# Kernel optimization log

Measured on AMD Instinct MI355X. Metric: run time of the kernel, lower is better.

## Reference

```python
import jax, jax.numpy as jnp
import numpy as np

B, P, R, H, M, A = 2048, 2048, 4096, 6, 256, 256
TAU, BETA = 0.1, 5.0


def setup_inputs() -> dict:
    key = jax.random.key(0)
    ks = jax.random.split(key, 12)
    M_minus = jax.random.uniform(ks[0], (B, M), dtype=jnp.float32)
    # rank-0 actions as sparse binary mask over predicates
    action_mask = (jax.random.uniform(ks[1], (B, P)) < 0.01).astype(jnp.float32)
    # temporal gate per (microstep, rule): 0/1
    gate = (jax.random.uniform(ks[2], (B, R)) < 0.7).astype(jnp.float32)
    body_idx = jax.random.randint(ks[3], (R, H), 0, P, dtype=jnp.int32)
    body_mask = (jax.random.uniform(ks[4], (R, H)) < 0.6).astype(jnp.float32)
    body_mask = body_mask.at[:, 0].set(1.0)  # every rule has >=1 body atom
    head_idx = jax.random.randint(ks[5], (R,), 0, P, dtype=jnp.int32)
    mental_pos = jnp.arange(M, dtype=jnp.int32)  # mental predicates occupy first M slots
    rtype = jax.random.randint(ks[6], (R,), 0, 3)
    is_toM = (rtype <= 1).astype(jnp.float32)   # A->M or M->M rules
    is_toA = (rtype == 2).astype(jnp.float32)   # M->A rules
    Gamma_AtoM = 0.1 * jax.random.normal(ks[7], (R, M), dtype=jnp.float32)
    Gamma_MtoA = 0.1 * jax.random.normal(ks[8], (R, A), dtype=jnp.float32)
    b = -2.0 * jnp.ones((A,), dtype=jnp.float32)
    w = 0.2 * jax.random.normal(ks[9], (A, M), dtype=jnp.float32)
    return {"M_minus": M_minus, "action_mask": action_mask, "gate": gate,
            "body_mask": body_mask, "is_toM": is_toM, "is_toA": is_toA,
            "Gamma_AtoM": Gamma_AtoM, "Gamma_MtoA": Gamma_MtoA, "b": b, "w": w,
            "body_idx": body_idx, "head_idx": head_idx, "mental_pos": mental_pos}


def reference(M_minus, action_mask, gate, body_mask, is_toM, is_toA,
              Gamma_AtoM, Gamma_MtoA, b, w, body_idx, head_idx, mental_pos):
    Mclip = jnp.clip(M_minus, 0.0, 1.0)                       # [B,M]
    # build_val_for_microstep: scatter mental vals, set rank-0 actions to 1
    val = jnp.zeros((B, P), dtype=M_minus.dtype).at[:, mental_pos].set(Mclip)
    val = jnp.maximum(val, action_mask)                        # [B,P]

    # eval_clause_exact: soft-AND (soft-min, temperature tau) over body atoms
    body_vals = val[:, body_idx]                               # [B,R,H] gather
    v = jnp.where(body_mask > 0, body_vals, 1e4)               # padded slots never min
    g_body = -TAU * jax.nn.logsumexp(-v / TAU, axis=-1)        # [B,R]
    g = g_body * gate                                          # temporal gate

    # per-head clause aggregation: g_head = (1/beta) logsumexp_{r:head(r)=p} beta*g_r
    def seg_lse(gb):  # gb: [R]
        mx = jax.ops.segment_max(BETA * gb, head_idx, num_segments=P)
        mx_safe = jnp.where(mx > -1e30, mx, 0.0)
        s = jax.ops.segment_sum(jnp.exp(BETA * gb - mx_safe[head_idx]),
                                head_idx, num_segments=P)
        lse = (mx_safe + jnp.log(jnp.maximum(s, 1e-30))) / BETA
        return jnp.where(s > 0, lse, -1e9)
    g_head = jax.vmap(seg_lse)(g)                              # [B,P]

    mental_mask = jnp.zeros((P,), dtype=val.dtype).at[mental_pos].set(1.0)
    val_new = jnp.where(mental_mask > 0, jnp.maximum(val, g_head), val)

    # S_j(t) = relu(sum over A->M/M->M rules gamma_AtoM[r] * g_r)
    S = jax.nn.relu(jnp.einsum('br,rm->bm', g * is_toM, Gamma_AtoM))  # [B,M]
    # lambda_k(t) = softplus(b + w@M) + relu(sum over M->A rules gamma_MtoA[r]*g_r)
    lam_ment = jax.nn.softplus(b + Mclip @ w.T)                # [B,A]
    lam_logic = jax.nn.relu(jnp.einsum('br,ra->ba', g * is_toA, Gamma_MtoA))
    lam = lam_ment + lam_logic
    return jnp.concatenate([val_new, S, lam], axis=-1)         # [B, P+M+A]
```

## Files before the change

### kernel.cpp

```cpp
#include <hip/hip_runtime.h>

typedef __attribute__((ext_vector_type(8))) short short8;
typedef __attribute__((ext_vector_type(4))) float f32x4;

#define B_DIM 2048
#define P_DIM 2048
#define R_DIM 4096
#define H_DIM 6
#define M_DIM 256
#define A_DIM 256
#define OUT_STRIDE 2560
#define NB 2

#define C1 14.426950408889634f
#define K2 0.06931471805599453f
#define C2 7.213475204444817f
#define K3 0.13862943611198906f

static __device__ __forceinline__ float fexp2(float x) { return __builtin_amdgcn_exp2f(x); }
static __device__ __forceinline__ float flog2(float x) { return __builtin_amdgcn_logf(x); }

static __device__ __forceinline__ unsigned short f2bf(float f) {
    unsigned u = __builtin_bit_cast(unsigned, f);
    u += 0x7fffu + ((u >> 16) & 1u);
    return (unsigned short)(u >> 16);
}
static __device__ __forceinline__ float bf2f_lo(unsigned u) {
    return __builtin_bit_cast(float, u << 16);
}
static __device__ __forceinline__ float bf2f_hi(unsigned u) {
    return __builtin_bit_cast(float, u & 0xFFFF0000u);
}
static __device__ __forceinline__ unsigned short f2h(float f) {
    return __builtin_bit_cast(unsigned short, (_Float16)f);
}
static __device__ __forceinline__ float h2f(unsigned short u) {
    return (float)__builtin_bit_cast(_Float16, u);
}

__global__ __launch_bounds__(256) void prep_meta(
    const int* __restrict__ bidx, const float* __restrict__ bmask,
    const int* __restrict__ hidx, uint4* __restrict__ meta)
{
    const int r = blockIdx.x * 256 + threadIdx.x;
    const int* bi = bidx + r * H_DIM;
    const float* bm = bmask + r * H_DIM;
    unsigned s[H_DIM];
    #pragma unroll
    for (int h = 0; h < H_DIM; h++)
        s[h] = (bm[h] > 0.0f) ? (unsigned)bi[h] : 2048u;
    const int hh = hidx[r];
    unsigned sh = (hh < M_DIM) ? (unsigned)hh : 0xFFFFu;
    uint4 m;
    m.x = s[0] | (s[1] << 16);
    m.y = s[2] | (s[3] << 16);
    m.z = s[4] | (s[5] << 16);
    m.w = sh;
    meta[r] = m;
}

__global__ __launch_bounds__(1024, 8) void main_fused(
    const float* __restrict__ M_minus, const float* __restrict__ amask,
    const float* __restrict__ gate,    const uint4* __restrict__ meta,
    const float* __restrict__ GA, const float* __restrict__ GB,
    const float* __restrict__ isM, const float* __restrict__ isA,
    const float* __restrict__ w,
    unsigned short* __restrict__ GAT, unsigned short* __restrict__ GBT,
    unsigned short* __restrict__ wb,
    unsigned short* __restrict__ g_bf, unsigned short* __restrict__ mclip_bf,
    float* __restrict__ outp)
{
    __shared__ __align__(16) union SM {
        struct {
            unsigned vrowu[2052];
            float shead[NB][M_DIM];
        } mf;
        float prep[4][32][33];
    } sm;
    const int bid = blockIdx.x;
    const int tid = threadIdx.x;
    const int b0 = bid * NB;

    if (bid < 576) {
        const int s = tid >> 8, lt = tid & 255;
        const int u = bid * 4 + s;
        const int tx = lt & 31, ty = lt >> 5;
        if (u < 2048) {
            const int which = u >> 10;
            const int rem = u & 1023;
            const float* src = which ? GB : GA;
            const float* scv = which ? isA : isM;
            const int r0 = (rem >> 3) * 32;
            const int n0 = (rem & 7) * 32;
            #pragma unroll
            for (int q = 0; q < 4; q++) {
                int rr = ty + q * 8;
                sm.prep[s][rr][tx] = scv[r0 + rr] * src[(size_t)(r0 + rr) * 256 + n0 + tx];
            }
        } else {
            const int i = (u - 2048) * 256 + lt;
            wb[i] = f2bf(w[i]);
        }
        __syncthreads();
        if (u < 2048) {
            const int which = u >> 10;
            const int rem = u & 1023;
            unsigned short* dst = which ? GBT : GAT;
            const int r0 = (rem >> 3) * 32;
            const int n0 = (rem & 7) * 32;
            #pragma unroll
            for (int q = 0; q < 4; q++) {
                int nn = ty + q * 8;
                dst[(size_t)(n0 + nn) * R_DIM + r0 + tx] = f2bf(sm.prep[s][tx][nn]);
            }
        }
        __syncthreads();
    }

    if (tid < NB * M_DIM) sm.mf.shead[tid >> 8][tid & 255] = 0.0f;
    if (tid == 0) {
        unsigned sb = (unsigned)f2bf(-1.0e9f);
        sm.mf.vrowu[2048] = sb | (sb << 16);
    }

    {
        const int p0 = tid * 2;
        float2 a0 = *(const float2*)(amask + (size_t)b0 * P_DIM + p0);
        float2 a1 = *(const float2*)(amask + (size_t)(b0 + 1) * P_DIM + p0);
        if (tid < M_DIM / 2) {
            float2 m0 = *(const float2*)(M_minus + (size_t)b0 * M_DIM + p0);
            float2 m1 = *(const float2*)(M_minus + (size_t)(b0 + 1) * M_DIM + p0);
            float mc00 = fminf(fmaxf(m0.x, 0.0f), 1.0f);
            float mc01 = fminf(fmaxf(m0.y, 0.0f), 1.0f);
            float mc10 = fminf(fmaxf(m1.x, 0.0f), 1.0f);
            float mc11 = fminf(fmaxf(m1.y, 0.0f), 1.0f);
            ushort2 w0; w0.x = f2bf(mc00); w0.y = f2bf(mc01);
            ushort2 w1; w1.x = f2bf(mc10); w1.y = f2bf(mc11);
            *(ushort2*)(mclip_bf + (size_t)b0 * M_DIM + p0) = w0;
            *(ushort2*)(mclip_bf + (size_t)(b0 + 1) * M_DIM + p0) = w1;
            a0.x = fmaxf(mc00, a0.x); a0.y = fmaxf(mc01, a0.y);
            a1.x = fmaxf(mc10, a1.x); a1.y = fmaxf(mc11, a1.y);
        }
        unsigned u0 = (unsigned)f2bf(-C1 * a0.x) | ((unsigned)f2bf(-C1 * a1.x) << 16);
        unsigned u1 = (unsigned)f2bf(-C1 * a0.y) | ((unsigned)f2bf(-C1 * a1.y) << 16);
        *(uint2*)&sm.mf.vrowu[p0] = make_uint2(u0, u1);
    }
    __syncthreads();

    const float* g0p = gate + (size_t)b0 * R_DIM;
    const float* g1p = gate + (size_t)(b0 + 1) * R_DIM;
    unsigned short* o0p = g_bf + (size_t)b0 * R_DIM;
    unsigned short* o1p = g_bf + (size_t)(b0 + 1) * R_DIM;

    uint4 mc = meta[tid];
    float ga = g0p[tid], gb = g1p[tid];
    #pragma unroll
    for (int it = 0; it < R_DIM / 1024; it++) {
        const int rr = tid + it * 1024;
        uint4 mn = mc; float gan = ga, gbn = gb;
        if (it < R_DIM / 1024 - 1) {
            mn  = meta[rr + 1024];
            gan = g0p[rr + 1024];
            gbn = g1p[rr + 1024];
        }
        const int i0 = mc.x & 0xFFFF, i1 = mc.x >> 16;
        const int i2 = mc.y & 0xFFFF, i3 = mc.y >> 16;
        const int i4 = mc.z & 0xFFFF, i5 = mc.z >> 16;
        const int hh = mc.w & 0xFFFF;
        unsigned u0 = sm.mf.vrowu[i0], u1 = sm.mf.vrowu[i1], u2 = sm.mf.vrowu[i2];
        unsigned u3 = sm.mf.vrowu[i3], u4 = sm.mf.vrowu[i4], u5 = sm.mf.vrowu[i5];

        float s0 = fexp2(bf2f_lo(u0)) + fexp2(bf2f_lo(u1)) + fexp2(bf2f_lo(u2))
                 + fexp2(bf2f_lo(u3)) + fexp2(bf2f_lo(u4)) + fexp2(bf2f_lo(u5));
        float s1 = fexp2(bf2f_hi(u0)) + fexp2(bf2f_hi(u1)) + fexp2(bf2f_hi(u2))
                 + fexp2(bf2f_hi(u3)) + fexp2(bf2f_hi(u4)) + fexp2(bf2f_hi(u5));
        float gg0 = flog2(s0) * (-K2 * ga);
        float gg1 = flog2(s1) * (-K2 * gb);
        o0p[rr] = f2bf(gg0);
        o1p[rr] = f2bf(gg1);
        if (hh < M_DIM) {
            atomicAdd(&sm.mf.shead[0][hh], fexp2(gg0 * C2));
            atomicAdd(&sm.mf.shead[1][hh], fexp2(gg1 * C2));
        }
        mc = mn; ga = gan; gb = gbn;
    }
    __syncthreads();

    {
        const int p0 = tid * 2;
        uint2 uu = *(const uint2*)&sm.mf.vrowu[p0];
        float v00 = -K2 * bf2f_lo(uu.x), v10 = -K2 * bf2f_hi(uu.x);
        float v01 = -K2 * bf2f_lo(uu.y), v11 = -K2 * bf2f_hi(uu.y);
        if (tid < M_DIM / 2) {
            float s00 = sm.mf.shead[0][p0], s01 = sm.mf.shead[0][p0 + 1];
            float s10 = sm.mf.shead[1][p0], s11 = sm.mf.shead[1][p0 + 1];
            if (s00 > 0.0f) v00 = fmaxf(v00, K3 * flog2(s00));
            if (s01 > 0.0f) v01 = fmaxf(v01, K3 * flog2(s01));
            if (s10 > 0.0f) v10 = fmaxf(v10, K3 * flog2(s10));
            if (s11 > 0.0f) v11 = fmaxf(v11, K3 * flog2(s11));
        }
        *(float2*)(outp + (size_t)b0 * OUT_STRIDE + p0)       = make_float2(v00, v01);
        *(float2*)(outp + (size_t)(b0 + 1) * OUT_STRIDE + p0) = make_float2(v10, v11);
    }
}

__device__ __forceinline__ void stage16(unsigned short* lds,
                                        const unsigned short* gsrc,
                                        int K, int c)
{
    const int row = c >> 4, slot = c & 15;
    const int k8 = slot ^ (row & 15);
    __builtin_amdgcn_global_load_lds(
        (const __attribute__((address_space(1))) void*)(gsrc + (size_t)row * K + k8 * 8),
        (__attribute__((address_space(3))) void*)(lds + c * 8), 16, 0, 0);
}

__global__ __launch_bounds__(256) void gemm_all(
    const unsigned short* __restrict__ g_bf,
    const unsigned short* __restrict__ GAT,
    const unsigned short* __restrict__ mclip,
    const unsigned short* __restrict__ w_bf,
    unsigned short* __restrict__ mainp, unsigned short* __restrict__ lamp)
{
    __shared__ __align__(16) unsigned short Alds[128 * 128];
    __shared__ __align__(16) unsigned short Blds[64 * 128];
    const int bid = blockIdx.x;
    const int tid = threadIdx.x;
    const int lane = tid & 63, wid = tid >> 6;
    const int wr = wid >> 1, wc = wid & 1;

    if (bid < 512) {
        const int l = (bid & 7) * 64 + (bid >> 3);
        const int m0 = (l & 15) * 128;
        const int n0 = ((l >> 4) & 7) * 64;
        const int z  = l >> 7;
        const int K = R_DIM, Kc = R_DIM / 4, k0 = z * Kc, NS = 512;
        unsigned short* part = mainp + (size_t)z * B_DIM * NS;
        f32x4 acc[4][2] = {};

        for (int kt = 0; kt < Kc; kt += 128) {
            const unsigned short* Ab = g_bf + (size_t)m0 * K + k0 + kt;
            const unsigned short* Bb = GAT  + (size_t)n0 * K + k0 + kt;
            #pragma unroll
            for (int q = 0; q < 8; q++) stage16(Alds, Ab, K, tid + q * 256);
            #pragma unroll
            for (int q = 0; q < 4; q++) stage16(Blds, Bb, K, tid + q * 256);
            __syncthreads();
            #pragma unroll
            for (int ks = 0; ks < 4; ks++) {
                const int k8 = ks * 4 + (lane >> 4);
                const int ra = wr * 64 + (lane & 15);
                const int rb = wc * 32 + (lane & 15);
                const int sa = (k8 ^ (ra & 15)) << 3;
                const int sb = (k8 ^ (rb & 15)) << 3;
                short8 a0 = *(const short8*)&Alds[(ra)      * 128 + sa];
                short8 a1 = *(const short8*)&Alds[(ra + 16) * 128 + sa];
                short8 a2 = *(const short8*)&Alds[(ra + 32) * 128 + sa];
                short8 a3 = *(const short8*)&Alds[(ra + 48) * 128 + sa];
                short8 b0 = *(const short8*)&Blds[(rb)      * 128 + sb];
                short8 b1 = *(const short8*)&Blds[(rb + 16) * 128 + sb];
                acc[0][0] = __builtin_amdgcn_mfma_f32_16x16x32_bf16(a0, b0, acc[0][0], 0, 0, 0);
                acc[0][1] = __builtin_amdgcn_mfma_f32_16x16x32_bf16(a0, b1, acc[0][1], 0, 0, 0);
                acc[1][0] = __builtin_amdgcn_mfma_f32_16x16x32_bf16(a1, b0, acc[1][0], 0, 0, 0);
                acc[1][1] = __builtin_amdgcn_mfma_f32_16x16x32_bf16(a1, b1, acc[1][1], 0, 0, 0);
                acc[2][0] = __builtin_amdgcn_mfma_f32_16x16x32_bf16(a2, b0, acc[2][0], 0, 0, 0);
                acc[2][1] = __builtin_amdgcn_mfma_f32_16x16x32_bf16(a2, b1, acc[2][1], 0, 0, 0);
                acc[3][0] = __builtin_amdgcn_mfma_f32_16x16x32_bf16(a3, b0, acc[3][0], 0, 0, 0);
                acc[3][1] = __builtin_amdgcn_mfma_f32_16x16x32_bf16(a3, b1, acc[3][1], 0, 0, 0);
            }
            __syncthreads();
        }
        const int rbase = (lane >> 4) * 4;
        const int cbase = lane & 15;
        #pragma unroll
        for (int i = 0; i < 4; i++) {
            #pragma unroll
            for (int j = 0; j < 2; j++) {
                const int gn = n0 + wc * 32 + j * 16 + cbase;
                #pragma unroll
                for (int q = 0; q < 4; q++) {
                    const int gm = m0 + wr * 64 + i * 16 + rbase + q;
                    part[(size_t)gm * NS + gn] = f2h(acc[i][j][q]);
                }
            }
        }
    } else {
        const int l = bid - 512;
        const int m0 = (l & 31) * 64;
        const int n0 = ((l >> 5) & 3) * 64;
        const int z  = l >> 7;
        const int K = M_DIM, Kc = M_DIM / 2, k0 = z * Kc, NS = A_DIM;
        unsigned short* part = lamp + (size_t)z * B_DIM * NS;
        f32x4 acc[2][2] = {};

        const unsigned short* Ab = mclip + (size_t)m0 * K + k0;
        const unsigned short* Bb = w_bf  + (size_t)n0 * K + k0;
        #pragma unroll
        for (int q = 0; q < 4; q++) {
            stage16(Alds, Ab, K, tid + q * 256);
            stage16(Blds, Bb, K, tid + q * 256);
        }
        __syncthreads();
        #pragma unroll
        for (int ks = 0; ks < 4; ks++) {
            const int k8 = ks * 4 + (lane >> 4);
            const int r0a = wr * 32 + (lane & 15);
            const int r0b = wc * 32 + (lane & 15);
            const int sa = (k8 ^ (r0a & 15)) << 3;
            const int sb = (k8 ^ (r0b & 15)) << 3;
            short8 a0 = *(const short8*)&Alds[(r0a)      * 128 + sa];
            short8 a1 = *(const short8*)&Alds[(r0a + 16) * 128 + sa];
            short8 b0 = *(const short8*)&Blds[(r0b)      * 128 + sb];
            short8 b1 = *(const short8*)&Blds[(r0b + 16) * 128 + sb];
            acc[0][0] = __builtin_amdgcn_mfma_f32_16x16x32_bf16(a0, b0, acc[0][0], 0, 0, 0);
            acc[0][1] = __builtin_amdgcn_mfma_f32_16x16x32_bf16(a0, b1, acc[0][1], 0, 0, 0);
            acc[1][0] = __builtin_amdgcn_mfma_f32_16x16x32_bf16(a1, b0, acc[1][0], 0, 0, 0);
            acc[1][1] = __builtin_amdgcn_mfma_f32_16x16x32_bf16(a1, b1, acc[1][1], 0, 0, 0);
        }
        const int rbase = (lane >> 4) * 4;
        const int cbase = lane & 15;
        #pragma unroll
        for (int i = 0; i < 2; i++) {
            #pragma unroll
            for (int j = 0; j < 2; j++) {
                const int gn = n0 + wc * 32 + j * 16 + cbase;
                #pragma unroll
                for (int q = 0; q < 4; q++) {
                    const int gm = m0 + wr * 32 + i * 16 + rbase + q;
                    part[(size_t)gm * NS + gn] = f2h(acc[i][j][q]);
                }
            }
        }
    }
}

__global__ __launch_bounds__(256) void epilogue(
    const unsigned short* __restrict__ mainpart,
    const unsigned short* __restrict__ lampart,
    const float* __restrict__ bvec, float* __restrict__ outp)
{
    const int idx = blockIdx.x * 256 + threadIdx.x;
    const int m = idx >> 7, n4 = idx & 127;
    const size_t mb = (size_t)m * 128 + n4;
    const size_t zs = (size_t)B_DIM * 128;
    float sx = 0.0f, sy = 0.0f, sz = 0.0f, sw = 0.0f;
    #pragma unroll
    for (int z = 0; z < 4; z++) {
        ushort4 t = ((const ushort4*)mainpart)[mb + z * zs];
        sx += h2f(t.x); sy += h2f(t.y); sz += h2f(t.z); sw += h2f(t.w);
    }
    sx = fmaxf(sx, 0.0f); sy = fmaxf(sy, 0.0f);
    sz = fmaxf(sz, 0.0f); sw = fmaxf(sw, 0.0f);
    if (n4 >= 64) {
        const int na = n4 - 64;
        const size_t lb = (size_t)m * 64 + na;
        const size_t ls = (size_t)B_DIM * 64;
        ushort4 u0 = ((const ushort4*)lampart)[lb];
        ushort4 u1 = ((const ushort4*)lampart)[lb + ls];
        float4 bb = ((const float4*)bvec)[na];
        float x0 = bb.x + h2f(u0.x) + h2f(u1.x);
        float x1 = bb.y + h2f(u0.y) + h2f(u1.y);
        float x2 = bb.z + h2f(u0.z) + h2f(u1.z);
        float x3 = bb.w + h2f(u0.w) + h2f(u1.w);
        sx += (x0 > 20.0f) ? x0 : log1pf(__expf(x0));
        sy += (x1 > 20.0f) ? x1 : log1pf(__expf(x1));
        sz += (x2 > 20.0f) ? x2 : log1pf(__expf(x2));
        sw += (x3 > 20.0f) ? x3 : log1pf(__expf(x3));
    }
    float4 s; s.x = sx; s.y = sy; s.z = sz; s.w = sw;
    ((float4*)(outp + (size_t)m * OUT_STRIDE + 2048))[n4] = s;
}

extern "C" void kernel_launch(void* const* d_in, const int* in_sizes, int n_in,
                              void* d_out, int out_size, void* d_ws, size_t ws_size,
                              hipStream_t stream)
{
    const float* M_minus = (const float*)d_in[0];
    const float* amask   = (const float*)d_in[1];
    const float* gate    = (const float*)d_in[2];
    const float* bmask   = (const float*)d_in[3];
    const float* isM     = (const float*)d_in[4];
    const float* isA     = (const float*)d_in[5];
    const float* GA      = (const float*)d_in[6];
    const float* GB      = (const float*)d_in[7];
    const float* bvec    = (const float*)d_in[8];
    const float* w       = (const float*)d_in[9];
    const int*   bidx    = (const int*)d_in[10];
    const int*   hidx    = (const int*)d_in[11];
    float* outp = (float*)d_out;

    char* ws = (char*)d_ws;
    unsigned short* g_bf   = (unsigned short*)(ws + 0);
    unsigned short* GAT    = (unsigned short*)(ws + (16u<<20));
    unsigned short* GBT    = (unsigned short*)(ws + (18u<<20));
    unsigned short* w_bf   = (unsigned short*)(ws + (20u<<20));
    uint4*          meta   = (uint4*)(ws + (20u<<20) + (256u<<10));
    unsigned short* mclip  = (unsigned short*)(ws + (21u<<20));
    unsigned short* mainp  = (unsigned short*)(ws + (22u<<20));
    unsigned short* lamp   = (unsigned short*)(ws + (38u<<20));

    prep_meta<<<dim3(R_DIM / 256), dim3(256), 0, stream>>>(bidx, bmask, hidx, meta);
    main_fused<<<dim3(B_DIM / NB), dim3(1024), 0, stream>>>(
        M_minus, amask, gate, meta, GA, GB, isM, isA, w,
        GAT, GBT, w_bf, g_bf, mclip, outp);
    gemm_all<<<dim3(768), dim3(256), 0, stream>>>(
        g_bf, GAT, mclip, w_bf, mainp, lamp);
    epilogue<<<dim3((B_DIM * 128) / 256), dim3(256), 0, stream>>>(
        mainp, lamp, bvec, outp);
}
```

Baseline: 49.63 us.

## Process four batch rows per block in fused clause kernel

Each block of the fused kernel now handles four batch rows instead of two. The per-predicate values for all four rows are packed into a uint2 in LDS, so one gather per body atom serves four rows, and the meta index loads are shared across more rows. The grid halves to 512 blocks, so the GA/GB transpose prep now runs in every block and the w conversion moves to the first 64 blocks. The cost is more register pressure and fewer blocks to spread across the CUs.

```diff
diff --git a/kernel.cpp b/kernel.cpp
--- a/kernel.cpp
+++ b/kernel.cpp
@@ -10,7 +10,7 @@
 #define M_DIM 256
 #define A_DIM 256
 #define OUT_STRIDE 2560
-#define NB 2
+#define NB 4
 
 #define C1 14.426950408889634f
 #define K2 0.06931471805599453f
@@ -72,7 +72,7 @@
 {
     __shared__ __align__(16) union SM {
         struct {
-            unsigned vrowu[2052];
+            uint2 vrowu4[2052];
             float shead[NB][M_DIM];
         } mf;
         float prep[4][32][33];
@@ -81,38 +81,31 @@
     const int tid = threadIdx.x;
     const int b0 = bid * NB;
 
-    if (bid < 576) {
+    {
         const int s = tid >> 8, lt = tid & 255;
         const int u = bid * 4 + s;
         const int tx = lt & 31, ty = lt >> 5;
-        if (u < 2048) {
-            const int which = u >> 10;
-            const int rem = u & 1023;
-            const float* src = which ? GB : GA;
-            const float* scv = which ? isA : isM;
-            const int r0 = (rem >> 3) * 32;
-            const int n0 = (rem & 7) * 32;
-            #pragma unroll
-            for (int q = 0; q < 4; q++) {
-                int rr = ty + q * 8;
-                sm.prep[s][rr][tx] = scv[r0 + rr] * src[(size_t)(r0 + rr) * 256 + n0 + tx];
-            }
-        } else {
-            const int i = (u - 2048) * 256 + lt;
+        const int which = u >> 10;
+        const int rem = u & 1023;
+        const float* src = which ? GB : GA;
+        const float* scv = which ? isA : isM;
+        const int r0 = (rem >> 3) * 32;
+        const int n0 = (rem & 7) * 32;
+        #pragma unroll
+        for (int q = 0; q < 4; q++) {
+            int rr = ty + q * 8;
+            sm.prep[s][rr][tx] = scv[r0 + rr] * src[(size_t)(r0 + rr) * 256 + n0 + tx];
+        }
+        __syncthreads();
+        unsigned short* dst = which ? GBT : GAT;
+        #pragma unroll
+        for (int q = 0; q < 4; q++) {
+            int nn = ty + q * 8;
+            dst[(size_t)(n0 + nn) * R_DIM + r0 + tx] = f2bf(sm.prep[s][tx][nn]);
+        }
+        if (bid < 64) {
+            const int i = bid * 1024 + tid;
             wb[i] = f2bf(w[i]);
-        }
-        __syncthreads();
-        if (u < 2048) {
-            const int which = u >> 10;
-            const int rem = u & 1023;
-            unsigned short* dst = which ? GBT : GAT;
-            const int r0 = (rem >> 3) * 32;
-            const int n0 = (rem & 7) * 32;
-            #pragma unroll
-            for (int q = 0; q < 4; q++) {
-                int nn = ty + q * 8;
-                dst[(size_t)(n0 + nn) * R_DIM + r0 + tx] = f2bf(sm.prep[s][tx][nn]);
-            }
         }
         __syncthreads();
     }
@@ -120,87 +113,99 @@
     if (tid < NB * M_DIM) sm.mf.shead[tid >> 8][tid & 255] = 0.0f;
     if (tid == 0) {
         unsigned sb = (unsigned)f2bf(-1.0e9f);
-        sm.mf.vrowu[2048] = sb | (sb << 16);
+        sm.mf.vrowu4[2048] = make_uint2(sb | (sb << 16), sb | (sb << 16));
     }
 
     {
         const int p0 = tid * 2;
-        float2 a0 = *(const float2*)(amask + (size_t)b0 * P_DIM + p0);
-        float2 a1 = *(const float2*)(amask + (size_t)(b0 + 1) * P_DIM + p0);
+        float2 a[NB];
+        #pragma unroll
+        for (int r = 0; r < NB; r++)
+            a[r] = *(const float2*)(amask + (size_t)(b0 + r) * P_DIM + p0);
         if (tid < M_DIM / 2) {
-            float2 m0 = *(const float2*)(M_minus + (size_t)b0 * M_DIM + p0);
-            float2 m1 = *(const float2*)(M_minus + (size_t)(b0 + 1) * M_DIM + p0);
-            float mc00 = fminf(fmaxf(m0.x, 0.0f), 1.0f);
-            float mc01 = fminf(fmaxf(m0.y, 0.0f), 1.0f);
-            float mc10 = fminf(fmaxf(m1.x, 0.0f), 1.0f);
-            float mc11 = fminf(fmaxf(m1.y, 0.0f), 1.0f);
-            ushort2 w0; w0.x = f2bf(mc00); w0.y = f2bf(mc01);
-            ushort2 w1; w1.x = f2bf(mc10); w1.y = f2bf(mc11);
-            *(ushort2*)(mclip_bf + (size_t)b0 * M_DIM + p0) = w0;
-            *(ushort2*)(mclip_bf + (size_t)(b0 + 1) * M_DIM + p0) = w1;
-            a0.x = fmaxf(mc00, a0.x); a0.y = fmaxf(mc01, a0.y);
-            a1.x = fmaxf(mc10, a1.x); a1.y = fmaxf(mc11, a1.y);
-        }
-        unsigned u0 = (unsigned)f2bf(-C1 * a0.x) | ((unsigned)f2bf(-C1 * a1.x) << 16);
-        unsigned u1 = (unsigned)f2bf(-C1 * a0.y) | ((unsigned)f2bf(-C1 * a1.y) << 16);
-        *(uint2*)&sm.mf.vrowu[p0] = make_uint2(u0, u1);
+            #pragma unroll
+            for (int r = 0; r < NB; r++) {
+                float2 m = *(const float2*)(M_minus + (size_t)(b0 + r) * M_DIM + p0);
+                float mc0 = fminf(fmaxf(m.x, 0.0f), 1.0f);
+                float mc1 = fminf(fmaxf(m.y, 0.0f), 1.0f);
+                ushort2 wv; wv.x = f2bf(mc0); wv.y = f2bf(mc1);
+                *(ushort2*)(mclip_bf + (size_t)(b0 + r) * M_DIM + p0) = wv;
+                a[r].x = fmaxf(mc0, a[r].x);
+                a[r].y = fmaxf(mc1, a[r].y);
+            }
+        }
+        uint4 pk;
+        pk.x = (unsigned)f2bf(-C1 * a[0].x) | ((unsigned)f2bf(-C1 * a[1].x) << 16);
+        pk.y = (unsigned)f2bf(-C1 * a[2].x) | ((unsigned)f2bf(-C1 * a[3].x) << 16);
+        pk.z = (unsigned)f2bf(-C1 * a[0].y) | ((unsigned)f2bf(-C1 * a[1].y) << 16);
+        pk.w = (unsigned)f2bf(-C1 * a[2].y) | ((unsigned)f2bf(-C1 * a[3].y) << 16);
+        *(uint4*)&sm.mf.vrowu4[p0] = pk;
     }
     __syncthreads();
 
-    const float* g0p = gate + (size_t)b0 * R_DIM;
-    const float* g1p = gate + (size_t)(b0 + 1) * R_DIM;
-    unsigned short* o0p = g_bf + (size_t)b0 * R_DIM;
-    unsigned short* o1p = g_bf + (size_t)(b0 + 1) * R_DIM;
-
     uint4 mc = meta[tid];
-    float ga = g0p[tid], gb = g1p[tid];
     #pragma unroll
     for (int it = 0; it < R_DIM / 1024; it++) {
         const int rr = tid + it * 1024;
-        uint4 mn = mc; float gan = ga, gbn = gb;
-        if (it < R_DIM / 1024 - 1) {
-            mn  = meta[rr + 1024];
-            gan = g0p[rr + 1024];
-            gbn = g1p[rr + 1024];
-        }
+        uint4 mn = mc;
+        if (it < R_DIM / 1024 - 1) mn = meta[rr + 1024];
+        float gv[NB];
+        #pragma unroll
+        for (int r = 0; r < NB; r++)
+            gv[r] = gate[(size_t)(b0 + r) * R_DIM + rr];
         const int i0 = mc.x & 0xFFFF, i1 = mc.x >> 16;
         const int i2 = mc.y & 0xFFFF, i3 = mc.y >> 16;
         const int i4 = mc.z & 0xFFFF, i5 = mc.z >> 16;
         const int hh = mc.w & 0xFFFF;
-        unsigned u0 = sm.mf.vrowu[i0], u1 = sm.mf.vrowu[i1], u2 = sm.mf.vrowu[i2];
-        unsigned u3 = sm.mf.vrowu[i3], u4 = sm.mf.vrowu[i4], u5 = sm.mf.vrowu[i5];
-
-        float s0 = fexp2(bf2f_lo(u0)) + fexp2(bf2f_lo(u1)) + fexp2(bf2f_lo(u2))
-                 + fexp2(bf2f_lo(u3)) + fexp2(bf2f_lo(u4)) + fexp2(bf2f_lo(u5));
-        float s1 = fexp2(bf2f_hi(u0)) + fexp2(bf2f_hi(u1)) + fexp2(bf2f_hi(u2))
-                 + fexp2(bf2f_hi(u3)) + fexp2(bf2f_hi(u4)) + fexp2(bf2f_hi(u5));
-        float gg0 = flog2(s0) * (-K2 * ga);
-        float gg1 = flog2(s1) * (-K2 * gb);
-        o0p[rr] = f2bf(gg0);
-        o1p[rr] = f2bf(gg1);
+        uint2 u0 = sm.mf.vrowu4[i0], u1 = sm.mf.vrowu4[i1], u2 = sm.mf.vrowu4[i2];
+        uint2 u3 = sm.mf.vrowu4[i3], u4 = sm.mf.vrowu4[i4], u5 = sm.mf.vrowu4[i5];
+
+        float s0 = fexp2(bf2f_lo(u0.x)) + fexp2(bf2f_lo(u1.x)) + fexp2(bf2f_lo(u2.x))
+                 + fexp2(bf2f_lo(u3.x)) + fexp2(bf2f_lo(u4.x)) + fexp2(bf2f_lo(u5.x));
+        float s1 = fexp2(bf2f_hi(u0.x)) + fexp2(bf2f_hi(u1.x)) + fexp2(bf2f_hi(u2.x))
+                 + fexp2(bf2f_hi(u3.x)) + fexp2(bf2f_hi(u4.x)) + fexp2(bf2f_hi(u5.x));
+        float s2 = fexp2(bf2f_lo(u0.y)) + fexp2(bf2f_lo(u1.y)) + fexp2(bf2f_lo(u2.y))
+                 + fexp2(bf2f_lo(u3.y)) + fexp2(bf2f_lo(u4.y)) + fexp2(bf2f_lo(u5.y));
+        float s3 = fexp2(bf2f_hi(u0.y)) + fexp2(bf2f_hi(u1.y)) + fexp2(bf2f_hi(u2.y))
+                 + fexp2(bf2f_hi(u3.y)) + fexp2(bf2f_hi(u4.y)) + fexp2(bf2f_hi(u5.y));
+        float gg0 = flog2(s0) * (-K2 * gv[0]);
+        float gg1 = flog2(s1) * (-K2 * gv[1]);
+        float gg2 = flog2(s2) * (-K2 * gv[2]);
+        float gg3 = flog2(s3) * (-K2 * gv[3]);
+        g_bf[(size_t)b0 * R_DIM + rr]       = f2bf(gg0);
+        g_bf[(size_t)(b0 + 1) * R_DIM + rr] = f2bf(gg1);
+        g_bf[(size_t)(b0 + 2) * R_DIM + rr] = f2bf(gg2);
+        g_bf[(size_t)(b0 + 3) * R_DIM + rr] = f2bf(gg3);
         if (hh < M_DIM) {
             atomicAdd(&sm.mf.shead[0][hh], fexp2(gg0 * C2));
             atomicAdd(&sm.mf.shead[1][hh], fexp2(gg1 * C2));
-        }
-        mc = mn; ga = gan; gb = gbn;
+            atomicAdd(&sm.mf.shead[2][hh], fexp2(gg2 * C2));
+            atomicAdd(&sm.mf.shead[3][hh], fexp2(gg3 * C2));
+        }
+        mc = mn;
     }
     __syncthreads();
 
     {
         const int p0 = tid * 2;
-        uint2 uu = *(const uint2*)&sm.mf.vrowu[p0];
-        float v00 = -K2 * bf2f_lo(uu.x), v10 = -K2 * bf2f_hi(uu.x);
-        float v01 = -K2 * bf2f_lo(uu.y), v11 = -K2 * bf2f_hi(uu.y);
+        uint4 uu = *(const uint4*)&sm.mf.vrowu4[p0];
+        float v[NB][2];
+        v[0][0] = -K2 * bf2f_lo(uu.x); v[1][0] = -K2 * bf2f_hi(uu.x);
+        v[2][0] = -K2 * bf2f_lo(uu.y); v[3][0] = -K2 * bf2f_hi(uu.y);
+        v[0][1] = -K2 * bf2f_lo(uu.z); v[1][1] = -K2 * bf2f_hi(uu.z);
+        v[2][1] = -K2 * bf2f_lo(uu.w); v[3][1] = -K2 * bf2f_hi(uu.w);
         if (tid < M_DIM / 2) {
-            float s00 = sm.mf.shead[0][p0], s01 = sm.mf.shead[0][p0 + 1];
-            float s10 = sm.mf.shead[1][p0], s11 = sm.mf.shead[1][p0 + 1];
-            if (s00 > 0.0f) v00 = fmaxf(v00, K3 * flog2(s00));
-            if (s01 > 0.0f) v01 = fmaxf(v01, K3 * flog2(s01));
-            if (s10 > 0.0f) v10 = fmaxf(v10, K3 * flog2(s10));
-            if (s11 > 0.0f) v11 = fmaxf(v11, K3 * flog2(s11));
-        }
-        *(float2*)(outp + (size_t)b0 * OUT_STRIDE + p0)       = make_float2(v00, v01);
-        *(float2*)(outp + (size_t)(b0 + 1) * OUT_STRIDE + p0) = make_float2(v10, v11);
+            #pragma unroll
+            for (int r = 0; r < NB; r++) {
+                float sa = sm.mf.shead[r][p0], sb = sm.mf.shead[r][p0 + 1];
+                if (sa > 0.0f) v[r][0] = fmaxf(v[r][0], K3 * flog2(sa));
+                if (sb > 0.0f) v[r][1] = fmaxf(v[r][1], K3 * flog2(sb));
+            }
+        }
+        #pragma unroll
+        for (int r = 0; r < NB; r++)
+            *(float2*)(outp + (size_t)(b0 + r) * OUT_STRIDE + p0) =
+                make_float2(v[r][0], v[r][1]);
     }
 }
 
```

Result: faster. 48.14 us (-3.0%).
